# Optimization experiments

Hardware: AMD Instinct MI355X
Metric: run time of the kernel (lower is better)

## Reference

```python
import jax, jax.numpy as jnp
import numpy as np

HID = 1024       # hidden_size
H = 8            # num_attention_heads
KVH = 2          # num_key_value_heads
D = HID // H     # head_dim = 128
WINDOW = 2048    # sliding_window
THETA = 10000.0  # rope_theta
B, S = 1, 4096


def rotate_half(x):
    x1, x2 = jnp.split(x, 2, axis=-1)
    return jnp.concatenate([-x2, x1], axis=-1)


def setup_inputs() -> dict:
    key = jax.random.key(0)
    ks = jax.random.split(key, 5)
    scale = 0.02
    return {
        "hidden_states": jax.random.normal(ks[0], (B, S, HID), dtype=jnp.float32),
        "wq": jax.random.normal(ks[1], (H * D, HID), dtype=jnp.float32) * scale,
        "wk": jax.random.normal(ks[2], (KVH * D, HID), dtype=jnp.float32) * scale,
        "wv": jax.random.normal(ks[3], (KVH * D, HID), dtype=jnp.float32) * scale,
        "wo": jax.random.normal(ks[4], (HID, H * D), dtype=jnp.float32) * scale,
        "position_ids": jnp.broadcast_to(jnp.arange(S, dtype=jnp.int64 if jax.config.jax_enable_x64 else jnp.int32)[None, :], (B, S)),
    }


def reference(hidden_states, wq, wk, wv, wo, position_ids):
    b, s, _ = hidden_states.shape
    # projections (torch nn.Linear: x @ W^T)
    q = (hidden_states @ wq.T).reshape(b, s, H, D).transpose(0, 2, 1, 3)      # bhsd
    k = (hidden_states @ wk.T).reshape(b, s, KVH, D).transpose(0, 2, 1, 3)    # b(kv)sd
    v = (hidden_states @ wv.T).reshape(b, s, KVH, D).transpose(0, 2, 1, 3)

    # RoPE cache (head_dim, seq_len)
    inv_freq = 1.0 / THETA ** (jnp.arange(0, D, 2, dtype=jnp.float32) / D)
    t = jnp.arange(s, dtype=jnp.float32)
    freqs = t[:, None] * inv_freq[None, :]
    emb = jnp.concatenate([freqs, freqs], axis=-1)           # (S, D)
    cos = jnp.cos(emb)[position_ids][:, None]                # (B,1,S,D)
    sin = jnp.sin(emb)[position_ids][:, None]
    q = q * cos + rotate_half(q) * sin
    k = k * cos + rotate_half(k) * sin

    # GQA: repeat kv heads to match query heads (repeat_interleave on head dim)
    groups = H // KVH
    k = jnp.repeat(k, groups, axis=1)
    v = jnp.repeat(v, groups, axis=1)

    # full score matrix with sliding-window causal mask
    scores = jnp.einsum("bhqd,bhkd->bhqk", q, k)
    i = jnp.arange(s)[:, None]
    j = jnp.arange(s)[None, :]
    mask = (j <= i) & (j > i - WINDOW)                       # causal + window
    scores = jnp.where(mask[None, None], scores, -jnp.inf) / jnp.sqrt(jnp.float32(D))

    probs = jax.nn.softmax(scores.astype(jnp.float32), axis=-1).astype(q.dtype)
    ctx = jnp.einsum("bhqk,bhkd->bhqd", probs, v)
    ctx = ctx.transpose(0, 2, 1, 3).reshape(b, s, H * D)
    return ctx @ wo.T
```

## Files before the change

kernel.cpp:

```cpp
#include <hip/hip_runtime.h>

#define S_LEN 4096
#define HIDDEN 1024
#define NH 8
#define NKV 2
#define HD 128
#define WIN 2048

typedef short bf16x8 __attribute__((ext_vector_type(8)));
typedef short bf16x4 __attribute__((ext_vector_type(4)));
typedef float f32x4 __attribute__((ext_vector_type(4)));
typedef unsigned short u16x4 __attribute__((ext_vector_type(4)));

__device__ __forceinline__ unsigned short f2b(float f) {
    unsigned int u = __builtin_bit_cast(unsigned int, f);
    u += 0x7fffu + ((u >> 16) & 1u);
    return (unsigned short)(u >> 16);
}
__device__ __forceinline__ float b2f(unsigned short u) {
    unsigned int x = ((unsigned int)u) << 16;
    return __builtin_bit_cast(float, x);
}

__device__ __forceinline__ void gl_lds16(const unsigned short* g, unsigned short* l) {
    __builtin_amdgcn_global_load_lds(
        (const __attribute__((address_space(1))) unsigned int*)g,
        (__attribute__((address_space(3))) unsigned int*)l, 16, 0, 0);
}

#define WAIT_VM6   0x0F76
#define WAIT_VM0   0x0F70
#define MEMFENCE() __asm__ volatile("" ::: "memory")

__global__ __launch_bounds__(256) void cvt5(
    const float* __restrict__ s0, unsigned short* __restrict__ t0, int n0,
    const float* __restrict__ s1, unsigned short* __restrict__ t1, int n1,
    const float* __restrict__ s2, unsigned short* __restrict__ t2, int n2,
    const float* __restrict__ s3, unsigned short* __restrict__ t3, int n3,
    const float* __restrict__ s4, unsigned short* __restrict__ t4, int n4)
{
    int i = blockIdx.x * 256 + threadIdx.x;
    const float* s; unsigned short* t;
    if (i < n0)              { s = s0; t = t0; }
    else if ((i -= n0) < n1) { s = s1; t = t1; }
    else if ((i -= n1) < n2) { s = s2; t = t2; }
    else if ((i -= n2) < n3) { s = s3; t = t3; }
    else if ((i -= n3) < n4) { s = s4; t = t4; }
    else return;
    f32x4 v = *(const f32x4*)(s + (size_t)i * 4);
    u16x4 r = { f2b(v[0]), f2b(v[1]), f2b(v[2]), f2b(v[3]) };
    *(u16x4*)(t + (size_t)i * 4) = r;
}

__global__ __launch_bounds__(256, 2) void gemm128(
    const unsigned short* __restrict__ A, const unsigned short* __restrict__ W,
    float* __restrict__ Cf, unsigned short* __restrict__ Cb,
    int M, int N, int K)
{
    __shared__ alignas(16) unsigned short As[6][64 * 32];
    __shared__ alignas(16) unsigned short Bs[6][128 * 32];

    int lane = threadIdx.x & 63;
    int w = threadIdx.x >> 6;
    int l15 = lane & 15, quad = lane >> 4;

    int tiles_n = N >> 7;
    int bid = (int)blockIdx.x;
    int nb = (int)gridDim.x;
    int lb = bid;
    if ((nb & 7) == 0) {
        int c = nb >> 3;
        lb = (bid & 7) * c + (bid >> 3);
    }
    int mt0 = lb / tiles_n;
    int nt0 = lb - mt0 * tiles_n;

    size_t goffA;
    {
        int s = w * 64 + lane;
        int row = s >> 2, spos = s & 3;
        int kblk = spos ^ ((row >> 1) & 3);
        goffA = (size_t)(mt0 * 64 + row) * K + kblk * 8;
    }
    size_t goffB[2];
    #pragma unroll
    for (int is = 0; is < 2; ++is) {
        int s = w * 128 + is * 64 + lane;
        int row = s >> 2, spos = s & 3;
        int kblk = spos ^ ((row >> 1) & 3);
        goffB[is] = (size_t)(nt0 * 128 + row) * K + kblk * 8;
    }

    int arow0 = (w >> 1) * 32;
    int brow0 = (w & 1) * 64;
    int aoff[2], boff[4];
    #pragma unroll
    for (int t = 0; t < 2; ++t) {
        int ra = arow0 + t * 16 + l15;
        aoff[t] = (ra * 4 + (quad ^ ((ra >> 1) & 3))) * 8;
    }
    #pragma unroll
    for (int j = 0; j < 4; ++j) {
        int rb = brow0 + j * 16 + l15;
        boff[j] = (rb * 4 + (quad ^ ((rb >> 1) & 3))) * 8;
    }

    f32x4 acc[2][4];
    #pragma unroll
    for (int i = 0; i < 2; ++i)
        #pragma unroll
        for (int j = 0; j < 4; ++j) acc[i][j] = (f32x4){0.f, 0.f, 0.f, 0.f};

    auto stage = [&](int s, int b) {
        int k0 = s * 32;
        gl_lds16(A + goffA + k0, &As[b][(w * 64) * 8]);
        gl_lds16(W + goffB[0] + k0, &Bs[b][(w * 128 + 0) * 8]);
        gl_lds16(W + goffB[1] + k0, &Bs[b][(w * 128 + 64) * 8]);
    };

    int nk = K >> 5;
    int np = nk >> 1;
    if (nk > 0) stage(0, 0);
    if (nk > 1) stage(1, 1);
    if (nk > 2) stage(2, 2);
    if (nk > 3) stage(3, 3);
    int cb = 0, sb = 4;
    for (int j = 0; j < np; ++j) {
        MEMFENCE();
        if (j + 1 < np) __builtin_amdgcn_s_waitcnt(WAIT_VM6);
        else            __builtin_amdgcn_s_waitcnt(WAIT_VM0);
        __builtin_amdgcn_s_barrier();
        MEMFENCE();
        int s0 = 2 * j + 4;
        if (s0 < nk)     stage(s0, sb);
        if (s0 + 1 < nk) stage(s0 + 1, sb + 1 == 6 ? 0 : sb + 1);
        sb += 2; if (sb >= 6) sb -= 6;

        #pragma unroll
        for (int half = 0; half < 2; ++half) {
            const unsigned short* Ab = &As[cb + half][0];
            const unsigned short* Bb = &Bs[cb + half][0];
            bf16x8 af[2], bf_[4];
            #pragma unroll
            for (int t = 0; t < 2; ++t) af[t]  = *(const bf16x8*)(Ab + aoff[t]);
            #pragma unroll
            for (int jj = 0; jj < 4; ++jj) bf_[jj] = *(const bf16x8*)(Bb + boff[jj]);
            __builtin_amdgcn_s_setprio(1);
            #pragma unroll
            for (int i2 = 0; i2 < 2; ++i2)
                #pragma unroll
                for (int jj = 0; jj < 4; ++jj)
                    acc[i2][jj] = __builtin_amdgcn_mfma_f32_16x16x32_bf16(af[i2], bf_[jj], acc[i2][jj], 0, 0, 0);
            __builtin_amdgcn_s_setprio(0);
        }
        cb += 2; if (cb >= 6) cb -= 6;
        MEMFENCE();
    }

    #pragma unroll
    for (int i = 0; i < 2; ++i) {
        int row0 = mt0 * 64 + arow0 + i * 16 + quad * 4;
        #pragma unroll
        for (int j = 0; j < 4; ++j) {
            int col = nt0 * 128 + brow0 + j * 16 + l15;
            if (Cf) {
                #pragma unroll
                for (int reg = 0; reg < 4; ++reg)
                    Cf[(size_t)(row0 + reg) * N + col] = acc[i][j][reg];
            } else {
                #pragma unroll
                for (int reg = 0; reg < 4; ++reg)
                    Cb[(size_t)(row0 + reg) * N + col] = f2b(acc[i][j][reg]);
            }
        }
    }
}

#define QKVW (HIDDEN + 2 * NKV * HD)
__global__ __launch_bounds__(256, 2) void gemmqkv(
    const unsigned short* __restrict__ A, const unsigned short* __restrict__ W,
    const int* __restrict__ pos,
    unsigned short* __restrict__ Qb, unsigned short* __restrict__ Kb,
    unsigned short* __restrict__ Vt)
{
    __shared__ alignas(16) char pool[73728];
    unsigned short (*As)[64 * 32]  = (unsigned short (*)[64 * 32])(pool);
    unsigned short (*Bs)[128 * 32] = (unsigned short (*)[128 * 32])(pool + 24576);
    float (*Ex)[32][68] = (float (*)[32][68])(pool);
    unsigned short* T = (unsigned short*)(pool);

    int lane = threadIdx.x & 63;
    int w = threadIdx.x >> 6;
    int l15 = lane & 15, quad = lane >> 4;

    const int K = HIDDEN;
    int bid = (int)blockIdx.x;
    int lb = (bid & 7) * 96 + (bid >> 3);
    int mt0 = lb / 12;
    int nt0 = lb - mt0 * 12;

    size_t goffA;
    {
        int s = w * 64 + lane;
        int row = s >> 2, spos = s & 3;
        int kblk = spos ^ ((row >> 1) & 3);
        goffA = (size_t)(mt0 * 64 + row) * K + kblk * 8;
    }
    size_t goffB[2];
    #pragma unroll
    for (int is = 0; is < 2; ++is) {
        int s = w * 128 + is * 64 + lane;
        int row = s >> 2, spos = s & 3;
        int kblk = spos ^ ((row >> 1) & 3);
        goffB[is] = (size_t)(nt0 * 128 + row) * K + kblk * 8;
    }

    int arow0 = (w >> 1) * 32;
    int brow0 = (w & 1) * 64;
    int aoff[2], boff[4];
    #pragma unroll
    for (int t = 0; t < 2; ++t) {
        int ra = arow0 + t * 16 + l15;
        aoff[t] = (ra * 4 + (quad ^ ((ra >> 1) & 3))) * 8;
    }
    #pragma unroll
    for (int j = 0; j < 4; ++j) {
        int rb = brow0 + j * 16 + l15;
        boff[j] = (rb * 4 + (quad ^ ((rb >> 1) & 3))) * 8;
    }

    f32x4 acc[2][4];
    #pragma unroll
    for (int i = 0; i < 2; ++i)
        #pragma unroll
        for (int j = 0; j < 4; ++j) acc[i][j] = (f32x4){0.f, 0.f, 0.f, 0.f};

    auto stage = [&](int s, int b) {
        int k0 = s * 32;
        gl_lds16(A + goffA + k0, &As[b][(w * 64) * 8]);
        gl_lds16(W + goffB[0] + k0, &Bs[b][(w * 128 + 0) * 8]);
        gl_lds16(W + goffB[1] + k0, &Bs[b][(w * 128 + 64) * 8]);
    };

    stage(0, 0);
    stage(1, 1);
    stage(2, 2);
    stage(3, 3);
    int cb = 0, sb = 4;
    for (int j = 0; j < 16; ++j) {
        MEMFENCE();
        if (j < 15) __builtin_amdgcn_s_waitcnt(WAIT_VM6);
        else        __builtin_amdgcn_s_waitcnt(WAIT_VM0);
        __builtin_amdgcn_s_barrier();
        MEMFENCE();
        int s0 = 2 * j + 4;
        if (s0 < 32)     stage(s0, sb);
        if (s0 + 1 < 32) stage(s0 + 1, sb + 1 == 6 ? 0 : sb + 1);
        sb += 2; if (sb >= 6) sb -= 6;

        #pragma unroll
        for (int half = 0; half < 2; ++half) {
            const unsigned short* Ab = &As[cb + half][0];
            const unsigned short* Bb = &Bs[cb + half][0];
            bf16x8 af[2], bf_[4];
            #pragma unroll
            for (int t = 0; t < 2; ++t) af[t]  = *(const bf16x8*)(Ab + aoff[t]);
            #pragma unroll
            for (int jj = 0; jj < 4; ++jj) bf_[jj] = *(const bf16x8*)(Bb + boff[jj]);
            __builtin_amdgcn_s_setprio(1);
            #pragma unroll
            for (int i2 = 0; i2 < 2; ++i2)
                #pragma unroll
                for (int jj = 0; jj < 4; ++jj)
                    acc[i2][jj] = __builtin_amdgcn_mfma_f32_16x16x32_bf16(af[i2], bf_[jj], acc[i2][jj], 0, 0, 0);
            __builtin_amdgcn_s_setprio(0);
        }
        cb += 2; if (cb >= 6) cb -= 6;
        MEMFENCE();
    }

    if (nt0 >= 10) {
        int kv = nt0 - 10;
        __syncthreads();
        #pragma unroll
        for (int i = 0; i < 2; ++i) {
            int srow = arow0 + i * 16 + quad * 4;
            #pragma unroll
            for (int j = 0; j < 4; ++j) {
                int d = brow0 + j * 16 + l15;
                #pragma unroll
                for (int reg = 0; reg < 4; ++reg)
                    T[(srow + reg) * 130 + d] = f2b(acc[i][j][reg]);
            }
        }
        __syncthreads();
        int tid = threadIdx.x;
        int dl = tid >> 4;
        int s4 = (tid & 15) * 4;
        #pragma unroll
        for (int it = 0; it < 8; ++it) {
            int d = it * 16 + dl;
            u16x4 v4 = { T[(s4 + 0) * 130 + d], T[(s4 + 1) * 130 + d],
                         T[(s4 + 2) * 130 + d], T[(s4 + 3) * 130 + d] };
            *(u16x4*)(Vt + (size_t)kv * HD * S_LEN + (size_t)d * S_LEN
                      + mt0 * 64 + s4) = v4;
        }
        return;
    }

    bool isQ = (nt0 < 8);
    int kv = nt0 - 8;
    bool is64 = (pos[1] == 0) && (pos[3] == 0);
    const float qscale = 0.08838834764831843f;

    float invf[4];
    #pragma unroll
    for (int j = 0; j < 4; ++j) {
        int d6 = (brow0 + j * 16 + l15) & 63;
        invf[j] = exp2f(-(float)d6 * (13.287712379549449f / 64.0f));
    }

    __syncthreads();
    #pragma unroll
    for (int i = 0; i < 2; ++i)
        #pragma unroll
        for (int j = 0; j < 4; ++j)
            #pragma unroll
            for (int reg = 0; reg < 4; ++reg)
                Ex[w][i * 16 + quad * 4 + reg][j * 16 + l15] = acc[i][j][reg];
    __syncthreads();
    #pragma unroll
    for (int i = 0; i < 2; ++i) {
        #pragma unroll
        for (int reg = 0; reg < 4; ++reg) {
            int s = mt0 * 64 + arow0 + i * 16 + quad * 4 + reg;
            int pv_ = is64 ? pos[2 * s] : pos[s];
            float pf = (float)pv_;
            #pragma unroll
            for (int j = 0; j < 4; ++j) {
                float sn, cs;
                __sincosf(pf * invf[j], &sn, &cs);
                float a  = acc[i][j][reg];
                float pr = Ex[w ^ 1][i * 16 + quad * 4 + reg][j * 16 + l15];
                int d_local = brow0 + j * 16 + l15;
                float outv = (d_local < 64) ? (a * cs - pr * sn) : (a * cs + pr * sn);
                if (isQ) {
                    Qb[(size_t)s * HIDDEN + nt0 * HD + d_local] = f2b(outv * qscale);
                } else {
                    Kb[(size_t)kv * S_LEN * HD + (size_t)s * HD + d_local] = f2b(outv);
                }
            }
        }
    }
}

__global__ __launch_bounds__(256, 2) void attn_coop(
    const unsigned short* __restrict__ Qb, const unsigned short* __restrict__ Kb,
    const unsigned short* __restrict__ Vt, unsigned short* __restrict__ Ctx)
{
    __shared__ alignas(16) unsigned short Klds[2][64 * 128];
    __shared__ alignas(16) unsigned short Vlds[2][128 * 64];

    int lane = threadIdx.x & 63;
    int w = threadIdx.x >> 6;
    int l15 = lane & 15, quad = lane >> 4;
    int h = blockIdx.y;
    int kv = h >> 2;
    int qt = (h & 4) ? (63 - (int)blockIdx.x) : (int)blockIdx.x;
    int qb = qt * 64;
    int q16 = qb + w * 16;

    bf16x8 a_q[4];
    const unsigned short* qrow = Qb + (size_t)(q16 + l15) * HIDDEN + h * HD + quad * 8;
    #pragma unroll
    for (int st = 0; st < 4; ++st) a_q[st] = *(const bf16x8*)(qrow + st * 32);

    bf16x4 ones4;
    #pragma unroll
    for (int i = 0; i < 4; ++i) ones4[i] = (short)0x3F80;

    int lo = qb - (WIN - 1); if (lo < 0) lo = 0; lo &= ~63;
    int nch = (qb + 64 - lo) >> 6;

    const unsigned short* gbase;
    unsigned short* ldsdst[2];
    int myoff[8];
    int jmul;
    if (w < 2) {
        gbase = Kb + (size_t)kv * S_LEN * HD;
        ldsdst[0] = &Klds[0][w * 8 * 512];
        ldsdst[1] = &Klds[1][w * 8 * 512];
        jmul = HD;
        #pragma unroll
        for (int tt = 0; tt < 8; ++tt) {
            int t = w * 8 + tt;
            int key  = t * 4 + (lane >> 4);
            int dblk = (lane & 15) ^ (key & 15);
            myoff[tt] = key * HD + dblk * 8;
        }
    } else {
        gbase = Vt + (size_t)kv * HD * S_LEN;
        ldsdst[0] = &Vlds[0][(w - 2) * 8 * 512];
        ldsdst[1] = &Vlds[1][(w - 2) * 8 * 512];
        jmul = 1;
        #pragma unroll
        for (int tt = 0; tt < 8; ++tt) {
            int t = (w - 2) * 8 + tt;
            int d    = t * 8 + (lane >> 3);
            int kblk = (lane & 7) ^ (d & 7);
            myoff[tt] = d * S_LEN + kblk * 8;
        }
    }

    auto issue = [&](int c) {
        int j0 = lo + c * 64;
        const unsigned short* src = gbase + (size_t)j0 * jmul;
        unsigned short* dst = ldsdst[c & 1];
        #pragma unroll
        for (int tt = 0; tt < 8; ++tt)
            gl_lds16(src + myoff[tt], dst + tt * 512);
    };

    f32x4 o[9];
    #pragma unroll
    for (int nd = 0; nd < 9; ++nd) o[nd] = (f32x4){0.f, 0.f, 0.f, 0.f};

    issue(0);

    for (int c = 0; c < nch; ++c) {
        int j0 = lo + c * 64;

        MEMFENCE();
        __builtin_amdgcn_s_waitcnt(WAIT_VM0);
        __builtin_amdgcn_s_barrier();
        MEMFENCE();
        if (c + 1 < nch) issue(c + 1);

        const unsigned short* Kc = &Klds[c & 1][0];
        const unsigned short* Vc = &Vlds[c & 1][0];

        f32x4 sc[4];
        #pragma unroll
        for (int t = 0; t < 4; ++t) {
            sc[t] = (f32x4){0.f, 0.f, 0.f, 0.f};
            int key = t * 16 + l15;
            #pragma unroll
            for (int st = 0; st < 4; ++st) {
                int off16 = key * 16 + ((st * 4 + quad) ^ (key & 15));
                bf16x8 ak = *(const bf16x8*)(Kc + off16 * 8);
                sc[t] = __builtin_amdgcn_mfma_f32_16x16x32_bf16(ak, a_q[st], sc[t], 0, 0, 0);
            }
        }

        float p[4][4];
        if (j0 + 63 <= q16 && j0 > q16 + 15 - WIN) {
            #pragma unroll
            for (int t = 0; t < 4; ++t)
                #pragma unroll
                for (int reg = 0; reg < 4; ++reg) p[t][reg] = __expf(sc[t][reg]);
        } else {
            int iq = q16 + l15;
            #pragma unroll
            for (int t = 0; t < 4; ++t) {
                #pragma unroll
                for (int reg = 0; reg < 4; ++reg) {
                    int key = j0 + t * 16 + quad * 4 + reg;
                    p[t][reg] = (key <= iq && key > iq - WIN) ? __expf(sc[t][reg]) : 0.f;
                }
            }
        }

        bf16x4 a_p[4];
        #pragma unroll
        for (int t = 0; t < 4; ++t) {
            a_p[t][0] = (short)f2b(p[t][0]);
            a_p[t][1] = (short)f2b(p[t][1]);
            a_p[t][2] = (short)f2b(p[t][2]);
            a_p[t][3] = (short)f2b(p[t][3]);
        }

        #pragma unroll
        for (int t = 0; t < 4; ++t) {
            #pragma unroll
            for (int nd = 0; nd < 8; ++nd) {
                int d = nd * 16 + l15;
                int kblk = t * 2 + (quad >> 1);
                int slot = d * 8 + (kblk ^ (d & 7));
                bf16x4 bv = *(const bf16x4*)(Vc + slot * 8 + (quad & 1) * 4);
                o[nd] = __builtin_amdgcn_mfma_f32_16x16x16bf16_1k(a_p[t], bv, o[nd], 0, 0, 0);
            }
            o[8] = __builtin_amdgcn_mfma_f32_16x16x16bf16_1k(a_p[t], ones4, o[8], 0, 0, 0);
        }
        MEMFENCE();
    }

    #pragma unroll
    for (int nd = 0; nd < 8; ++nd) {
        int d = nd * 16 + l15;
        #pragma unroll
        for (int reg = 0; reg < 4; ++reg) {
            int q = q16 + quad * 4 + reg;
            Ctx[(size_t)q * HIDDEN + h * HD + d] = f2b(o[nd][reg] / o[8][reg]);
        }
    }
}

extern "C" void kernel_launch(void* const* d_in, const int* in_sizes, int n_in,
                              void* d_out, int out_size, void* d_ws, size_t ws_size,
                              hipStream_t stream)
{
    const float* hidden = (const float*)d_in[0];
    const float* wq = (const float*)d_in[1];
    const float* wk = (const float*)d_in[2];
    const float* wv = (const float*)d_in[3];
    const float* wo = (const float*)d_in[4];
    const int* pos = (const int*)d_in[5];
    float* out = (float*)d_out;

    char* ws = (char*)d_ws;
    size_t off = 0;
    unsigned short* Hb   = (unsigned short*)(ws + off); off += (size_t)S_LEN * HIDDEN * 2;
    unsigned short* Wqkv = (unsigned short*)(ws + off); off += (size_t)QKVW * HIDDEN * 2;
    unsigned short* Wob  = (unsigned short*)(ws + off); off += (size_t)HIDDEN * HIDDEN * 2;
    unsigned short* Qb   = (unsigned short*)(ws + off); off += (size_t)S_LEN * HIDDEN * 2;
    unsigned short* Kb   = (unsigned short*)(ws + off); off += (size_t)S_LEN * NKV * HD * 2;
    unsigned short* Vt   = (unsigned short*)(ws + off); off += (size_t)S_LEN * NKV * HD * 2;
    unsigned short* Cb   = (unsigned short*)(ws + off); off += (size_t)S_LEN * HIDDEN * 2;

    const int n_h  = S_LEN * HIDDEN / 4;
    const int n_wq = HIDDEN * HIDDEN / 4;
    const int n_wk = NKV * HD * HIDDEN / 4;
    int tot4 = n_h + n_wq + 2 * n_wk + n_wq;
    cvt5<<<(tot4 + 255) / 256, 256, 0, stream>>>(
        hidden, Hb, n_h,
        wq, Wqkv, n_wq,
        wk, Wqkv + (size_t)HIDDEN * HIDDEN, n_wk,
        wv, Wqkv + (size_t)(HIDDEN + NKV * HD) * HIDDEN, n_wk,
        wo, Wob, n_wq);

    gemmqkv<<<(S_LEN / 64) * 12, 256, 0, stream>>>(
        Hb, Wqkv, pos, Qb, Kb, Vt);

    attn_coop<<<dim3(S_LEN / 64, NH), 256, 0, stream>>>(Qb, Kb, Vt, Cb);

    gemm128<<<(S_LEN / 64) * (HIDDEN / 128), 256, 0, stream>>>(
        Cb, Wob, out, nullptr, S_LEN, HIDDEN, HIDDEN);
}
```

Measured before the change: 180.2 us.

## Fuse all four kernels into one persistent kernel with grid-wide barriers

```diff
diff --git a/kernel.cpp b/kernel.cpp
--- a/kernel.cpp
+++ b/kernel.cpp
@@ -32,475 +32,472 @@
 #define WAIT_VM0   0x0F70
 #define MEMFENCE() __asm__ volatile("" ::: "memory")
 
-__global__ __launch_bounds__(256) void cvt5(
-    const float* __restrict__ s0, unsigned short* __restrict__ t0, int n0,
-    const float* __restrict__ s1, unsigned short* __restrict__ t1, int n1,
-    const float* __restrict__ s2, unsigned short* __restrict__ t2, int n2,
-    const float* __restrict__ s3, unsigned short* __restrict__ t3, int n3,
-    const float* __restrict__ s4, unsigned short* __restrict__ t4, int n4)
+#define NBLK 512
+
+__device__ __forceinline__ void gsync(unsigned int* cnt) {
+    __syncthreads();
+    if (threadIdx.x == 0) {
+        __threadfence();
+        atomicAdd(cnt, 1u);
+        while (atomicAdd(cnt, 0u) < (unsigned)NBLK)
+            __builtin_amdgcn_s_sleep(2);
+        __threadfence();
+    }
+    __syncthreads();
+}
+
+#define QKVW (HIDDEN + 2 * NKV * HD)
+__global__ __launch_bounds__(256, 2) void fused(
+    const float* __restrict__ hidden, const float* __restrict__ wq,
+    const float* __restrict__ wk, const float* __restrict__ wv,
+    const float* __restrict__ wo, const int* __restrict__ pos,
+    unsigned short* __restrict__ Hb, unsigned short* __restrict__ Wqkv,
+    unsigned short* __restrict__ Wob, unsigned short* __restrict__ Qb,
+    unsigned short* __restrict__ Kb, unsigned short* __restrict__ Vt,
+    unsigned short* __restrict__ Cb, float* __restrict__ out,
+    unsigned int* __restrict__ sync)
 {
-    int i = blockIdx.x * 256 + threadIdx.x;
-    const float* s; unsigned short* t;
-    if (i < n0)              { s = s0; t = t0; }
-    else if ((i -= n0) < n1) { s = s1; t = t1; }
-    else if ((i -= n1) < n2) { s = s2; t = t2; }
-    else if ((i -= n2) < n3) { s = s3; t = t3; }
-    else if ((i -= n3) < n4) { s = s4; t = t4; }
-    else return;
-    f32x4 v = *(const f32x4*)(s + (size_t)i * 4);
-    u16x4 r = { f2b(v[0]), f2b(v[1]), f2b(v[2]), f2b(v[3]) };
-    *(u16x4*)(t + (size_t)i * 4) = r;
-}
-
-__global__ __launch_bounds__(256, 2) void gemm128(
-    const unsigned short* __restrict__ A, const unsigned short* __restrict__ W,
-    float* __restrict__ Cf, unsigned short* __restrict__ Cb,
-    int M, int N, int K)
-{
-    __shared__ alignas(16) unsigned short As[6][64 * 32];
-    __shared__ alignas(16) unsigned short Bs[6][128 * 32];
-
+    __shared__ alignas(16) char pool[73728];
+
+    int bid = (int)blockIdx.x;
     int lane = threadIdx.x & 63;
     int w = threadIdx.x >> 6;
     int l15 = lane & 15, quad = lane >> 4;
 
-    int tiles_n = N >> 7;
-    int bid = (int)blockIdx.x;
-    int nb = (int)gridDim.x;
-    int lb = bid;
-    if ((nb & 7) == 0) {
-        int c = nb >> 3;
-        lb = (bid & 7) * c + (bid >> 3);
+    {
+        const int n_h  = S_LEN * HIDDEN / 4;
+        const int n_wq = HIDDEN * HIDDEN / 4;
+        const int n_wk = NKV * HD * HIDDEN / 4;
+        const int tot4 = n_h + n_wq + 2 * n_wk + n_wq;
+        for (int i0 = bid * 256 + (int)threadIdx.x; i0 < tot4; i0 += NBLK * 256) {
+            int i = i0;
+            const float* s; unsigned short* t;
+            if (i < n_h)              { s = hidden; t = Hb; }
+            else if ((i -= n_h) < n_wq) { s = wq; t = Wqkv; }
+            else if ((i -= n_wq) < n_wk) { s = wk; t = Wqkv + (size_t)HIDDEN * HIDDEN; }
+            else if ((i -= n_wk) < n_wk) { s = wv; t = Wqkv + (size_t)(HIDDEN + NKV * HD) * HIDDEN; }
+            else { i -= n_wk; s = wo; t = Wob; }
+            f32x4 v = *(const f32x4*)(s + (size_t)i * 4);
+            u16x4 r = { f2b(v[0]), f2b(v[1]), f2b(v[2]), f2b(v[3]) };
+            *(u16x4*)(t + (size_t)i * 4) = r;
+        }
     }
-    int mt0 = lb / tiles_n;
-    int nt0 = lb - mt0 * tiles_n;
-
-    size_t goffA;
+    gsync(&sync[0]);
+
     {
-        int s = w * 64 + lane;
-        int row = s >> 2, spos = s & 3;
-        int kblk = spos ^ ((row >> 1) & 3);
-        goffA = (size_t)(mt0 * 64 + row) * K + kblk * 8;
+        unsigned short (*As)[64 * 32]  = (unsigned short (*)[64 * 32])(pool);
+        unsigned short (*Bs)[128 * 32] = (unsigned short (*)[128 * 32])(pool + 24576);
+        float (*Ex)[32][68] = (float (*)[32][68])(pool);
+        unsigned short* T = (unsigned short*)(pool);
+
+        const int K = HIDDEN;
+        int arow0 = (w >> 1) * 32;
+        int brow0 = (w & 1) * 64;
+        int aoff[2], boff[4];
+        #pragma unroll
+        for (int t = 0; t < 2; ++t) {
+            int ra = arow0 + t * 16 + l15;
+            aoff[t] = (ra * 4 + (quad ^ ((ra >> 1) & 3))) * 8;
+        }
+        #pragma unroll
+        for (int j = 0; j < 4; ++j) {
+            int rb = brow0 + j * 16 + l15;
+            boff[j] = (rb * 4 + (quad ^ ((rb >> 1) & 3))) * 8;
+        }
+        const float qscale = 0.08838834764831843f;
+        bool is64 = (pos[1] == 0) && (pos[3] == 0);
+
+        for (int tile = bid; tile < 768; tile += NBLK) {
+            __syncthreads();
+            int lb = (tile & 7) * 96 + (tile >> 3);
+            int mt0 = lb / 12;
+            int nt0 = lb - mt0 * 12;
+
+            size_t goffA;
+            {
+                int s = w * 64 + lane;
+                int row = s >> 2, spos = s & 3;
+                int kblk = spos ^ ((row >> 1) & 3);
+                goffA = (size_t)(mt0 * 64 + row) * K + kblk * 8;
+            }
+            size_t goffB[2];
+            #pragma unroll
+            for (int is = 0; is < 2; ++is) {
+                int s = w * 128 + is * 64 + lane;
+                int row = s >> 2, spos = s & 3;
+                int kblk = spos ^ ((row >> 1) & 3);
+                goffB[is] = (size_t)(nt0 * 128 + row) * K + kblk * 8;
+            }
+
+            f32x4 acc[2][4];
+            #pragma unroll
+            for (int i = 0; i < 2; ++i)
+                #pragma unroll
+                for (int j = 0; j < 4; ++j) acc[i][j] = (f32x4){0.f, 0.f, 0.f, 0.f};
+
+            auto stage = [&](int s, int b) {
+                int k0 = s * 32;
+                gl_lds16(Hb + goffA + k0, &As[b][(w * 64) * 8]);
+                gl_lds16(Wqkv + goffB[0] + k0, &Bs[b][(w * 128 + 0) * 8]);
+                gl_lds16(Wqkv + goffB[1] + k0, &Bs[b][(w * 128 + 64) * 8]);
+            };
+
+            stage(0, 0);
+            stage(1, 1);
+            stage(2, 2);
+            stage(3, 3);
+            int cb = 0, sb = 4;
+            for (int j = 0; j < 16; ++j) {
+                MEMFENCE();
+                if (j < 15) __builtin_amdgcn_s_waitcnt(WAIT_VM6);
+                else        __builtin_amdgcn_s_waitcnt(WAIT_VM0);
+                __builtin_amdgcn_s_barrier();
+                MEMFENCE();
+                int s0 = 2 * j + 4;
+                if (s0 < 32)     stage(s0, sb);
+                if (s0 + 1 < 32) stage(s0 + 1, sb + 1 == 6 ? 0 : sb + 1);
+                sb += 2; if (sb >= 6) sb -= 6;
+
+                #pragma unroll
+                for (int half = 0; half < 2; ++half) {
+                    const unsigned short* Ab = &As[cb + half][0];
+                    const unsigned short* Bb = &Bs[cb + half][0];
+                    bf16x8 af[2], bf_[4];
+                    #pragma unroll
+                    for (int t = 0; t < 2; ++t) af[t]  = *(const bf16x8*)(Ab + aoff[t]);
+                    #pragma unroll
+                    for (int jj = 0; jj < 4; ++jj) bf_[jj] = *(const bf16x8*)(Bb + boff[jj]);
+                    __builtin_amdgcn_s_setprio(1);
+                    #pragma unroll
+                    for (int i2 = 0; i2 < 2; ++i2)
+                        #pragma unroll
+                        for (int jj = 0; jj < 4; ++jj)
+                            acc[i2][jj] = __builtin_amdgcn_mfma_f32_16x16x32_bf16(af[i2], bf_[jj], acc[i2][jj], 0, 0, 0);
+                    __builtin_amdgcn_s_setprio(0);
+                }
+                cb += 2; if (cb >= 6) cb -= 6;
+                MEMFENCE();
+            }
+
+            if (nt0 >= 10) {
+                int kv = nt0 - 10;
+                __syncthreads();
+                #pragma unroll
+                for (int i = 0; i < 2; ++i) {
+                    int srow = arow0 + i * 16 + quad * 4;
+                    #pragma unroll
+                    for (int j = 0; j < 4; ++j) {
+                        int d = brow0 + j * 16 + l15;
+                        #pragma unroll
+                        for (int reg = 0; reg < 4; ++reg)
+                            T[(srow + reg) * 130 + d] = f2b(acc[i][j][reg]);
+                    }
+                }
+                __syncthreads();
+                int tid = threadIdx.x;
+                int dl = tid >> 4;
+                int s4 = (tid & 15) * 4;
+                #pragma unroll
+                for (int it = 0; it < 8; ++it) {
+                    int d = it * 16 + dl;
+                    u16x4 v4 = { T[(s4 + 0) * 130 + d], T[(s4 + 1) * 130 + d],
+                                 T[(s4 + 2) * 130 + d], T[(s4 + 3) * 130 + d] };
+                    *(u16x4*)(Vt + (size_t)kv * HD * S_LEN + (size_t)d * S_LEN
+                              + mt0 * 64 + s4) = v4;
+                }
+            } else {
+                bool isQ = (nt0 < 8);
+                int kv = nt0 - 8;
+                float invf[4];
+                #pragma unroll
+                for (int j = 0; j < 4; ++j) {
+                    int d6 = (brow0 + j * 16 + l15) & 63;
+                    invf[j] = exp2f(-(float)d6 * (13.287712379549449f / 64.0f));
+                }
+                __syncthreads();
+                #pragma unroll
+                for (int i = 0; i < 2; ++i)
+                    #pragma unroll
+                    for (int j = 0; j < 4; ++j)
+                        #pragma unroll
+                        for (int reg = 0; reg < 4; ++reg)
+                            Ex[w][i * 16 + quad * 4 + reg][j * 16 + l15] = acc[i][j][reg];
+                __syncthreads();
+                #pragma unroll
+                for (int i = 0; i < 2; ++i) {
+                    #pragma unroll
+                    for (int reg = 0; reg < 4; ++reg) {
+                        int s = mt0 * 64 + arow0 + i * 16 + quad * 4 + reg;
+                        int pv_ = is64 ? pos[2 * s] : pos[s];
+                        float pf = (float)pv_;
+                        #pragma unroll
+                        for (int j = 0; j < 4; ++j) {
+                            float sn, cs;
+                            __sincosf(pf * invf[j], &sn, &cs);
+                            float a  = acc[i][j][reg];
+                            float pr = Ex[w ^ 1][i * 16 + quad * 4 + reg][j * 16 + l15];
+                            int d_local = brow0 + j * 16 + l15;
+                            float outv = (d_local < 64) ? (a * cs - pr * sn) : (a * cs + pr * sn);
+                            if (isQ) {
+                                Qb[(size_t)s * HIDDEN + nt0 * HD + d_local] = f2b(outv * qscale);
+                            } else {
+                                Kb[(size_t)kv * S_LEN * HD + (size_t)s * HD + d_local] = f2b(outv);
+                            }
+                        }
+                    }
+                }
+            }
+        }
     }
-    size_t goffB[2];
-    #pragma unroll
-    for (int is = 0; is < 2; ++is) {
-        int s = w * 128 + is * 64 + lane;
-        int row = s >> 2, spos = s & 3;
-        int kblk = spos ^ ((row >> 1) & 3);
-        goffB[is] = (size_t)(nt0 * 128 + row) * K + kblk * 8;
+    gsync(&sync[1]);
+
+    {
+        unsigned short (*Klds)[64 * 128] = (unsigned short (*)[64 * 128])(pool);
+        unsigned short (*Vlds)[128 * 64] = (unsigned short (*)[128 * 64])(pool + 32768);
+
+        int h = bid >> 6;
+        int bx = bid & 63;
+        int kv = h >> 2;
+        int qt = (h & 4) ? (63 - bx) : bx;
+        int qb = qt * 64;
+        int q16 = qb + w * 16;
+
+        bf16x8 a_q[4];
+        const unsigned short* qrow = Qb + (size_t)(q16 + l15) * HIDDEN + h * HD + quad * 8;
+        #pragma unroll
+        for (int st = 0; st < 4; ++st) a_q[st] = *(const bf16x8*)(qrow + st * 32);
+
+        bf16x4 ones4;
+        #pragma unroll
+        for (int i = 0; i < 4; ++i) ones4[i] = (short)0x3F80;
+
+        int lo = qb - (WIN - 1); if (lo < 0) lo = 0; lo &= ~63;
+        int nch = (qb + 64 - lo) >> 6;
+
+        const unsigned short* gbase;
+        unsigned short* ldsdst[2];
+        int myoff[8];
+        int jmul;
+        if (w < 2) {
+            gbase = Kb + (size_t)kv * S_LEN * HD;
+            ldsdst[0] = &Klds[0][w * 8 * 512];
+            ldsdst[1] = &Klds[1][w * 8 * 512];
+            jmul = HD;
+            #pragma unroll
+            for (int tt = 0; tt < 8; ++tt) {
+                int t = w * 8 + tt;
+                int key  = t * 4 + (lane >> 4);
+                int dblk = (lane & 15) ^ (key & 15);
+                myoff[tt] = key * HD + dblk * 8;
+            }
+        } else {
+            gbase = Vt + (size_t)kv * HD * S_LEN;
+            ldsdst[0] = &Vlds[0][(w - 2) * 8 * 512];
+            ldsdst[1] = &Vlds[1][(w - 2) * 8 * 512];
+            jmul = 1;
+            #pragma unroll
+            for (int tt = 0; tt < 8; ++tt) {
+                int t = (w - 2) * 8 + tt;
+                int d    = t * 8 + (lane >> 3);
+                int kblk = (lane & 7) ^ (d & 7);
+                myoff[tt] = d * S_LEN + kblk * 8;
+            }
+        }
+
+        auto issue = [&](int c) {
+            int j0 = lo + c * 64;
+            const unsigned short* src = gbase + (size_t)j0 * jmul;
+            unsigned short* dst = ldsdst[c & 1];
+            #pragma unroll
+            for (int tt = 0; tt < 8; ++tt)
+                gl_lds16(src + myoff[tt], dst + tt * 512);
+        };
+
+        f32x4 o[9];
+        #pragma unroll
+        for (int nd = 0; nd < 9; ++nd) o[nd] = (f32x4){0.f, 0.f, 0.f, 0.f};
+
+        issue(0);
+
+        for (int c = 0; c < nch; ++c) {
+            int j0 = lo + c * 64;
+
+            MEMFENCE();
+            __builtin_amdgcn_s_waitcnt(WAIT_VM0);
+            __builtin_amdgcn_s_barrier();
+            MEMFENCE();
+            if (c + 1 < nch) issue(c + 1);
+
+            const unsigned short* Kc = &Klds[c & 1][0];
+            const unsigned short* Vc = &Vlds[c & 1][0];
+
+            f32x4 sc[4];
+            #pragma unroll
+            for (int t = 0; t < 4; ++t) {
+                sc[t] = (f32x4){0.f, 0.f, 0.f, 0.f};
+                int key = t * 16 + l15;
+                #pragma unroll
+                for (int st = 0; st < 4; ++st) {
+                    int off16 = key * 16 + ((st * 4 + quad) ^ (key & 15));
+                    bf16x8 ak = *(const bf16x8*)(Kc + off16 * 8);
+                    sc[t] = __builtin_amdgcn_mfma_f32_16x16x32_bf16(ak, a_q[st], sc[t], 0, 0, 0);
+                }
+            }
+
+            float p[4][4];
+            if (j0 + 63 <= q16 && j0 > q16 + 15 - WIN) {
+                #pragma unroll
+                for (int t = 0; t < 4; ++t)
+                    #pragma unroll
+                    for (int reg = 0; reg < 4; ++reg) p[t][reg] = __expf(sc[t][reg]);
+            } else {
+                int iq = q16 + l15;
+                #pragma unroll
+                for (int t = 0; t < 4; ++t) {
+                    #pragma unroll
+                    for (int reg = 0; reg < 4; ++reg) {
+                        int key = j0 + t * 16 + quad * 4 + reg;
+                        p[t][reg] = (key <= iq && key > iq - WIN) ? __expf(sc[t][reg]) : 0.f;
+                    }
+                }
+            }
+
+            bf16x4 a_p[4];
+            #pragma unroll
+            for (int t = 0; t < 4; ++t) {
+                a_p[t][0] = (short)f2b(p[t][0]);
+                a_p[t][1] = (short)f2b(p[t][1]);
+                a_p[t][2] = (short)f2b(p[t][2]);
+                a_p[t][3] = (short)f2b(p[t][3]);
+            }
+
+            #pragma unroll
+            for (int t = 0; t < 4; ++t) {
+                #pragma unroll
+                for (int nd = 0; nd < 8; ++nd) {
+                    int d = nd * 16 + l15;
+                    int kblk = t * 2 + (quad >> 1);
+                    int slot = d * 8 + (kblk ^ (d & 7));
+                    bf16x4 bv = *(const bf16x4*)(Vc + slot * 8 + (quad & 1) * 4);
+                    o[nd] = __builtin_amdgcn_mfma_f32_16x16x16bf16_1k(a_p[t], bv, o[nd], 0, 0, 0);
+                }
+                o[8] = __builtin_amdgcn_mfma_f32_16x16x16bf16_1k(a_p[t], ones4, o[8], 0, 0, 0);
+            }
+            MEMFENCE();
+        }
+
+        #pragma unroll
+        for (int nd = 0; nd < 8; ++nd) {
+            int d = nd * 16 + l15;
+            #pragma unroll
+            for (int reg = 0; reg < 4; ++reg) {
+                int q = q16 + quad * 4 + reg;
+                Cb[(size_t)q * HIDDEN + h * HD + d] = f2b(o[nd][reg] / o[8][reg]);
+            }
+        }
     }
-
-    int arow0 = (w >> 1) * 32;
-    int brow0 = (w & 1) * 64;
-    int aoff[2], boff[4];
-    #pragma unroll
-    for (int t = 0; t < 2; ++t) {
-        int ra = arow0 + t * 16 + l15;
-        aoff[t] = (ra * 4 + (quad ^ ((ra >> 1) & 3))) * 8;
-    }
-    #pragma unroll
-    for (int j = 0; j < 4; ++j) {
-        int rb = brow0 + j * 16 + l15;
-        boff[j] = (rb * 4 + (quad ^ ((rb >> 1) & 3))) * 8;
-    }
-
-    f32x4 acc[2][4];
-    #pragma unroll
-    for (int i = 0; i < 2; ++i)
-        #pragma unroll
-        for (int j = 0; j < 4; ++j) acc[i][j] = (f32x4){0.f, 0.f, 0.f, 0.f};
-
-    auto stage = [&](int s, int b) {
-        int k0 = s * 32;
-        gl_lds16(A + goffA + k0, &As[b][(w * 64) * 8]);
-        gl_lds16(W + goffB[0] + k0, &Bs[b][(w * 128 + 0) * 8]);
-        gl_lds16(W + goffB[1] + k0, &Bs[b][(w * 128 + 64) * 8]);
-    };
-
-    int nk = K >> 5;
-    int np = nk >> 1;
-    if (nk > 0) stage(0, 0);
-    if (nk > 1) stage(1, 1);
-    if (nk > 2) stage(2, 2);
-    if (nk > 3) stage(3, 3);
-    int cb = 0, sb = 4;
-    for (int j = 0; j < np; ++j) {
-        MEMFENCE();
-        if (j + 1 < np) __builtin_amdgcn_s_waitcnt(WAIT_VM6);
-        else            __builtin_amdgcn_s_waitcnt(WAIT_VM0);
-        __builtin_amdgcn_s_barrier();
-        MEMFENCE();
-        int s0 = 2 * j + 4;
-        if (s0 < nk)     stage(s0, sb);
-        if (s0 + 1 < nk) stage(s0 + 1, sb + 1 == 6 ? 0 : sb + 1);
-        sb += 2; if (sb >= 6) sb -= 6;
-
-        #pragma unroll
-        for (int half = 0; half < 2; ++half) {
-            const unsigned short* Ab = &As[cb + half][0];
-            const unsigned short* Bb = &Bs[cb + half][0];
-            bf16x8 af[2], bf_[4];
-            #pragma unroll
-            for (int t = 0; t < 2; ++t) af[t]  = *(const bf16x8*)(Ab + aoff[t]);
-            #pragma unroll
-            for (int jj = 0; jj < 4; ++jj) bf_[jj] = *(const bf16x8*)(Bb + boff[jj]);
-            __builtin_amdgcn_s_setprio(1);
-            #pragma unroll
-            for (int i2 = 0; i2 < 2; ++i2)
-                #pragma unroll
-                for (int jj = 0; jj < 4; ++jj)
-                    acc[i2][jj] = __builtin_amdgcn_mfma_f32_16x16x32_bf16(af[i2], bf_[jj], acc[i2][jj], 0, 0, 0);
-            __builtin_amdgcn_s_setprio(0);
-        }
-        cb += 2; if (cb >= 6) cb -= 6;
-        MEMFENCE();
-    }
-
-    #pragma unroll
-    for (int i = 0; i < 2; ++i) {
-        int row0 = mt0 * 64 + arow0 + i * 16 + quad * 4;
+    gsync(&sync[2]);
+
+    {
+        unsigned short (*As)[64 * 32]  = (unsigned short (*)[64 * 32])(pool);
+        unsigned short (*Bs)[128 * 32] = (unsigned short (*)[128 * 32])(pool + 24576);
+
+        const int K = HIDDEN, N = HIDDEN;
+        int lb = (bid & 7) * 64 + (bid >> 3);
+        int mt0 = lb >> 3;
+        int nt0 = lb & 7;
+
+        size_t goffA;
+        {
+            int s = w * 64 + lane;
+            int row = s >> 2, spos = s & 3;
+            int kblk = spos ^ ((row >> 1) & 3);
+            goffA = (size_t)(mt0 * 64 + row) * K + kblk * 8;
+        }
+        size_t goffB[2];
+        #pragma unroll
+        for (int is = 0; is < 2; ++is) {
+            int s = w * 128 + is * 64 + lane;
+            int row = s >> 2, spos = s & 3;
+            int kblk = spos ^ ((row >> 1) & 3);
+            goffB[is] = (size_t)(nt0 * 128 + row) * K + kblk * 8;
+        }
+
+        int arow0 = (w >> 1) * 32;
+        int brow0 = (w & 1) * 64;
+        int aoff[2], boff[4];
+        #pragma unroll
+        for (int t = 0; t < 2; ++t) {
+            int ra = arow0 + t * 16 + l15;
+            aoff[t] = (ra * 4 + (quad ^ ((ra >> 1) & 3))) * 8;
+        }
         #pragma unroll
         for (int j = 0; j < 4; ++j) {
-            int col = nt0 * 128 + brow0 + j * 16 + l15;
-            if (Cf) {
+            int rb = brow0 + j * 16 + l15;
+            boff[j] = (rb * 4 + (quad ^ ((rb >> 1) & 3))) * 8;
+        }
+
+        f32x4 acc[2][4];
+        #pragma unroll
+        for (int i = 0; i < 2; ++i)
+            #pragma unroll
+            for (int j = 0; j < 4; ++j) acc[i][j] = (f32x4){0.f, 0.f, 0.f, 0.f};
+
+        auto stage = [&](int s, int b) {
+            int k0 = s * 32;
+            gl_lds16(Cb + goffA + k0, &As[b][(w * 64) * 8]);
+            gl_lds16(Wob + goffB[0] + k0, &Bs[b][(w * 128 + 0) * 8]);
+            gl_lds16(Wob + goffB[1] + k0, &Bs[b][(w * 128 + 64) * 8]);
+        };
+
+        __syncthreads();
+        stage(0, 0);
+        stage(1, 1);
+        stage(2, 2);
+        stage(3, 3);
+        int cb = 0, sb = 4;
+        for (int j = 0; j < 16; ++j) {
+            MEMFENCE();
+            if (j < 15) __builtin_amdgcn_s_waitcnt(WAIT_VM6);
+            else        __builtin_amdgcn_s_waitcnt(WAIT_VM0);
+            __builtin_amdgcn_s_barrier();
+            MEMFENCE();
+            int s0 = 2 * j + 4;
+            if (s0 < 32)     stage(s0, sb);
+            if (s0 + 1 < 32) stage(s0 + 1, sb + 1 == 6 ? 0 : sb + 1);
+            sb += 2; if (sb >= 6) sb -= 6;
+
+            #pragma unroll
+            for (int half = 0; half < 2; ++half) {
+                const unsigned short* Ab = &As[cb + half][0];
+                const unsigned short* Bb = &Bs[cb + half][0];
+                bf16x8 af[2], bf_[4];
+                #pragma unroll
+                for (int t = 0; t < 2; ++t) af[t]  = *(const bf16x8*)(Ab + aoff[t]);
+                #pragma unroll
+                for (int jj = 0; jj < 4; ++jj) bf_[jj] = *(const bf16x8*)(Bb + boff[jj]);
+                __builtin_amdgcn_s_setprio(1);
+                #pragma unroll
+                for (int i2 = 0; i2 < 2; ++i2)
+                    #pragma unroll
+                    for (int jj = 0; jj < 4; ++jj)
+                        acc[i2][jj] = __builtin_amdgcn_mfma_f32_16x16x32_bf16(af[i2], bf_[jj], acc[i2][jj], 0, 0, 0);
+                __builtin_amdgcn_s_setprio(0);
+            }
+            cb += 2; if (cb >= 6) cb -= 6;
+            MEMFENCE();
+        }
+
+        #pragma unroll
+        for (int i = 0; i < 2; ++i) {
+            int row0 = mt0 * 64 + arow0 + i * 16 + quad * 4;
+            #pragma unroll
+            for (int j = 0; j < 4; ++j) {
+                int col = nt0 * 128 + brow0 + j * 16 + l15;
                 #pragma unroll
                 for (int reg = 0; reg < 4; ++reg)
-                    Cf[(size_t)(row0 + reg) * N + col] = acc[i][j][reg];
-            } else {
-                #pragma unroll
-                for (int reg = 0; reg < 4; ++reg)
-                    Cb[(size_t)(row0 + reg) * N + col] = f2b(acc[i][j][reg]);
-            }
-        }
-    }
-}
-
-#define QKVW (HIDDEN + 2 * NKV * HD)
-__global__ __launch_bounds__(256, 2) void gemmqkv(
-    const unsigned short* __restrict__ A, const unsigned short* __restrict__ W,
-    const int* __restrict__ pos,
-    unsigned short* __restrict__ Qb, unsigned short* __restrict__ Kb,
-    unsigned short* __restrict__ Vt)
-{
-    __shared__ alignas(16) char pool[73728];
-    unsigned short (*As)[64 * 32]  = (unsigned short (*)[64 * 32])(pool);
-    unsigned short (*Bs)[128 * 32] = (unsigned short (*)[128 * 32])(pool + 24576);
-    float (*Ex)[32][68] = (float (*)[32][68])(pool);
-    unsigned short* T = (unsigned short*)(pool);
-
-    int lane = threadIdx.x & 63;
-    int w = threadIdx.x >> 6;
-    int l15 = lane & 15, quad = lane >> 4;
-
-    const int K = HIDDEN;
-    int bid = (int)blockIdx.x;
-    int lb = (bid & 7) * 96 + (bid >> 3);
-    int mt0 = lb / 12;
-    int nt0 = lb - mt0 * 12;
-
-    size_t goffA;
-    {
-        int s = w * 64 + lane;
-        int row = s >> 2, spos = s & 3;
-        int kblk = spos ^ ((row >> 1) & 3);
-        goffA = (size_t)(mt0 * 64 + row) * K + kblk * 8;
-    }
-    size_t goffB[2];
-    #pragma unroll
-    for (int is = 0; is < 2; ++is) {
-        int s = w * 128 + is * 64 + lane;
-        int row = s >> 2, spos = s & 3;
-        int kblk = spos ^ ((row >> 1) & 3);
-        goffB[is] = (size_t)(nt0 * 128 + row) * K + kblk * 8;
-    }
-
-    int arow0 = (w >> 1) * 32;
-    int brow0 = (w & 1) * 64;
-    int aoff[2], boff[4];
-    #pragma unroll
-    for (int t = 0; t < 2; ++t) {
-        int ra = arow0 + t * 16 + l15;
-        aoff[t] = (ra * 4 + (quad ^ ((ra >> 1) & 3))) * 8;
-    }
-    #pragma unroll
-    for (int j = 0; j < 4; ++j) {
-        int rb = brow0 + j * 16 + l15;
-        boff[j] = (rb * 4 + (quad ^ ((rb >> 1) & 3))) * 8;
-    }
-
-    f32x4 acc[2][4];
-    #pragma unroll
-    for (int i = 0; i < 2; ++i)
-        #pragma unroll
-        for (int j = 0; j < 4; ++j) acc[i][j] = (f32x4){0.f, 0.f, 0.f, 0.f};
-
-    auto stage = [&](int s, int b) {
-        int k0 = s * 32;
-        gl_lds16(A + goffA + k0, &As[b][(w * 64) * 8]);
-        gl_lds16(W + goffB[0] + k0, &Bs[b][(w * 128 + 0) * 8]);
-        gl_lds16(W + goffB[1] + k0, &Bs[b][(w * 128 + 64) * 8]);
-    };
-
-    stage(0, 0);
-    stage(1, 1);
-    stage(2, 2);
-    stage(3, 3);
-    int cb = 0, sb = 4;
-    for (int j = 0; j < 16; ++j) {
-        MEMFENCE();
-        if (j < 15) __builtin_amdgcn_s_waitcnt(WAIT_VM6);
-        else        __builtin_amdgcn_s_waitcnt(WAIT_VM0);
-        __builtin_amdgcn_s_barrier();
-        MEMFENCE();
-        int s0 = 2 * j + 4;
-        if (s0 < 32)     stage(s0, sb);
-        if (s0 + 1 < 32) stage(s0 + 1, sb + 1 == 6 ? 0 : sb + 1);
-        sb += 2; if (sb >= 6) sb -= 6;
-
-        #pragma unroll
-        for (int half = 0; half < 2; ++half) {
-            const unsigned short* Ab = &As[cb + half][0];
-            const unsigned short* Bb = &Bs[cb + half][0];
-            bf16x8 af[2], bf_[4];
-            #pragma unroll
-            for (int t = 0; t < 2; ++t) af[t]  = *(const bf16x8*)(Ab + aoff[t]);
-            #pragma unroll
-            for (int jj = 0; jj < 4; ++jj) bf_[jj] = *(const bf16x8*)(Bb + boff[jj]);
-            __builtin_amdgcn_s_setprio(1);
-            #pragma unroll
-            for (int i2 = 0; i2 < 2; ++i2)
-                #pragma unroll
-                for (int jj = 0; jj < 4; ++jj)
-                    acc[i2][jj] = __builtin_amdgcn_mfma_f32_16x16x32_bf16(af[i2], bf_[jj], acc[i2][jj], 0, 0, 0);
-            __builtin_amdgcn_s_setprio(0);
-        }
-        cb += 2; if (cb >= 6) cb -= 6;
-        MEMFENCE();
-    }
-
-    if (nt0 >= 10) {
-        int kv = nt0 - 10;
-        __syncthreads();
-        #pragma unroll
-        for (int i = 0; i < 2; ++i) {
-            int srow = arow0 + i * 16 + quad * 4;
-            #pragma unroll
-            for (int j = 0; j < 4; ++j) {
-                int d = brow0 + j * 16 + l15;
-                #pragma unroll
-                for (int reg = 0; reg < 4; ++reg)
-                    T[(srow + reg) * 130 + d] = f2b(acc[i][j][reg]);
-            }
-        }
-        __syncthreads();
-        int tid = threadIdx.x;
-        int dl = tid >> 4;
-        int s4 = (tid & 15) * 4;
-        #pragma unroll
-        for (int it = 0; it < 8; ++it) {
-            int d = it * 16 + dl;
-            u16x4 v4 = { T[(s4 + 0) * 130 + d], T[(s4 + 1) * 130 + d],
-                         T[(s4 + 2) * 130 + d], T[(s4 + 3) * 130 + d] };
-            *(u16x4*)(Vt + (size_t)kv * HD * S_LEN + (size_t)d * S_LEN
-                      + mt0 * 64 + s4) = v4;
-        }
-        return;
-    }
-
-    bool isQ = (nt0 < 8);
-    int kv = nt0 - 8;
-    bool is64 = (pos[1] == 0) && (pos[3] == 0);
-    const float qscale = 0.08838834764831843f;
-
-    float invf[4];
-    #pragma unroll
-    for (int j = 0; j < 4; ++j) {
-        int d6 = (brow0 + j * 16 + l15) & 63;
-        invf[j] = exp2f(-(float)d6 * (13.287712379549449f / 64.0f));
-    }
-
-    __syncthreads();
-    #pragma unroll
-    for (int i = 0; i < 2; ++i)
-        #pragma unroll
-        for (int j = 0; j < 4; ++j)
-            #pragma unroll
-            for (int reg = 0; reg < 4; ++reg)
-                Ex[w][i * 16 + quad * 4 + reg][j * 16 + l15] = acc[i][j][reg];
-    __syncthreads();
-    #pragma unroll
-    for (int i = 0; i < 2; ++i) {
-        #pragma unroll
-        for (int reg = 0; reg < 4; ++reg) {
-            int s = mt0 * 64 + arow0 + i * 16 + quad * 4 + reg;
-            int pv_ = is64 ? pos[2 * s] : pos[s];
-            float pf = (float)pv_;
-            #pragma unroll
-            for (int j = 0; j < 4; ++j) {
-                float sn, cs;
-                __sincosf(pf * invf[j], &sn, &cs);
-                float a  = acc[i][j][reg];
-                float pr = Ex[w ^ 1][i * 16 + quad * 4 + reg][j * 16 + l15];
-                int d_local = brow0 + j * 16 + l15;
-                float outv = (d_local < 64) ? (a * cs - pr * sn) : (a * cs + pr * sn);
-                if (isQ) {
-                    Qb[(size_t)s * HIDDEN + nt0 * HD + d_local] = f2b(outv * qscale);
-                } else {
-                    Kb[(size_t)kv * S_LEN * HD + (size_t)s * HD + d_local] = f2b(outv);
-                }
-            }
-        }
-    }
-}
-
-__global__ __launch_bounds__(256, 2) void attn_coop(
-    const unsigned short* __restrict__ Qb, const unsigned short* __restrict__ Kb,
-    const unsigned short* __restrict__ Vt, unsigned short* __restrict__ Ctx)
-{
-    __shared__ alignas(16) unsigned short Klds[2][64 * 128];
-    __shared__ alignas(16) unsigned short Vlds[2][128 * 64];
-
-    int lane = threadIdx.x & 63;
-    int w = threadIdx.x >> 6;
-    int l15 = lane & 15, quad = lane >> 4;
-    int h = blockIdx.y;
-    int kv = h >> 2;
-    int qt = (h & 4) ? (63 - (int)blockIdx.x) : (int)blockIdx.x;
-    int qb = qt * 64;
-    int q16 = qb + w * 16;
-
-    bf16x8 a_q[4];
-    const unsigned short* qrow = Qb + (size_t)(q16 + l15) * HIDDEN + h * HD + quad * 8;
-    #pragma unroll
-    for (int st = 0; st < 4; ++st) a_q[st] = *(const bf16x8*)(qrow + st * 32);
-
-    bf16x4 ones4;
-    #pragma unroll
-    for (int i = 0; i < 4; ++i) ones4[i] = (short)0x3F80;
-
-    int lo = qb - (WIN - 1); if (lo < 0) lo = 0; lo &= ~63;
-    int nch = (qb + 64 - lo) >> 6;
-
-    const unsigned short* gbase;
-    unsigned short* ldsdst[2];
-    int myoff[8];
-    int jmul;
-    if (w < 2) {
-        gbase = Kb + (size_t)kv * S_LEN * HD;
-        ldsdst[0] = &Klds[0][w * 8 * 512];
-        ldsdst[1] = &Klds[1][w * 8 * 512];
-        jmul = HD;
-        #pragma unroll
-        for (int tt = 0; tt < 8; ++tt) {
-            int t = w * 8 + tt;
-            int key  = t * 4 + (lane >> 4);
-            int dblk = (lane & 15) ^ (key & 15);
-            myoff[tt] = key * HD + dblk * 8;
-        }
-    } else {
-        gbase = Vt + (size_t)kv * HD * S_LEN;
-        ldsdst[0] = &Vlds[0][(w - 2) * 8 * 512];
-        ldsdst[1] = &Vlds[1][(w - 2) * 8 * 512];
-        jmul = 1;
-        #pragma unroll
-        for (int tt = 0; tt < 8; ++tt) {
-            int t = (w - 2) * 8 + tt;
-            int d    = t * 8 + (lane >> 3);
-            int kblk = (lane & 7) ^ (d & 7);
-            myoff[tt] = d * S_LEN + kblk * 8;
-        }
-    }
-
-    auto issue = [&](int c) {
-        int j0 = lo + c * 64;
-        const unsigned short* src = gbase + (size_t)j0 * jmul;
-        unsigned short* dst = ldsdst[c & 1];
-        #pragma unroll
-        for (int tt = 0; tt < 8; ++tt)
-            gl_lds16(src + myoff[tt], dst + tt * 512);
-    };
-
-    f32x4 o[9];
-    #pragma unroll
-    for (int nd = 0; nd < 9; ++nd) o[nd] = (f32x4){0.f, 0.f, 0.f, 0.f};
-
-    issue(0);
-
-    for (int c = 0; c < nch; ++c) {
-        int j0 = lo + c * 64;
-
-        MEMFENCE();
-        __builtin_amdgcn_s_waitcnt(WAIT_VM0);
-        __builtin_amdgcn_s_barrier();
-        MEMFENCE();
-        if (c + 1 < nch) issue(c + 1);
-
-        const unsigned short* Kc = &Klds[c & 1][0];
-        const unsigned short* Vc = &Vlds[c & 1][0];
-
-        f32x4 sc[4];
-        #pragma unroll
-        for (int t = 0; t < 4; ++t) {
-            sc[t] = (f32x4){0.f, 0.f, 0.f, 0.f};
-            int key = t * 16 + l15;
-            #pragma unroll
-            for (int st = 0; st < 4; ++st) {
-                int off16 = key * 16 + ((st * 4 + quad) ^ (key & 15));
-                bf16x8 ak = *(const bf16x8*)(Kc + off16 * 8);
-                sc[t] = __builtin_amdgcn_mfma_f32_16x16x32_bf16(ak, a_q[st], sc[t], 0, 0, 0);
-            }
-        }
-
-        float p[4][4];
-        if (j0 + 63 <= q16 && j0 > q16 + 15 - WIN) {
-            #pragma unroll
-            for (int t = 0; t < 4; ++t)
-                #pragma unroll
-                for (int reg = 0; reg < 4; ++reg) p[t][reg] = __expf(sc[t][reg]);
-        } else {
-            int iq = q16 + l15;
-            #pragma unroll
-            for (int t = 0; t < 4; ++t) {
-                #pragma unroll
-                for (int reg = 0; reg < 4; ++reg) {
-                    int key = j0 + t * 16 + quad * 4 + reg;
-                    p[t][reg] = (key <= iq && key > iq - WIN) ? __expf(sc[t][reg]) : 0.f;
-                }
-            }
-        }
-
-        bf16x4 a_p[4];
-        #pragma unroll
-        for (int t = 0; t < 4; ++t) {
-            a_p[t][0] = (short)f2b(p[t][0]);
-            a_p[t][1] = (short)f2b(p[t][1]);
-            a_p[t][2] = (short)f2b(p[t][2]);
-            a_p[t][3] = (short)f2b(p[t][3]);
-        }
-
-        #pragma unroll
-        for (int t = 0; t < 4; ++t) {
-            #pragma unroll
-            for (int nd = 0; nd < 8; ++nd) {
-                int d = nd * 16 + l15;
-                int kblk = t * 2 + (quad >> 1);
-                int slot = d * 8 + (kblk ^ (d & 7));
-                bf16x4 bv = *(const bf16x4*)(Vc + slot * 8 + (quad & 1) * 4);
-                o[nd] = __builtin_amdgcn_mfma_f32_16x16x16bf16_1k(a_p[t], bv, o[nd], 0, 0, 0);
-            }
-            o[8] = __builtin_amdgcn_mfma_f32_16x16x16bf16_1k(a_p[t], ones4, o[8], 0, 0, 0);
-        }
-        MEMFENCE();
-    }
-
-    #pragma unroll
-    for (int nd = 0; nd < 8; ++nd) {
-        int d = nd * 16 + l15;
-        #pragma unroll
-        for (int reg = 0; reg < 4; ++reg) {
-            int q = q16 + quad * 4 + reg;
-            Ctx[(size_t)q * HIDDEN + h * HD + d] = f2b(o[nd][reg] / o[8][reg]);
+                    out[(size_t)(row0 + reg) * N + col] = acc[i][j][reg];
+            }
         }
     }
 }
@@ -526,23 +523,11 @@
     unsigned short* Kb   = (unsigned short*)(ws + off); off += (size_t)S_LEN * NKV * HD * 2;
     unsigned short* Vt   = (unsigned short*)(ws + off); off += (size_t)S_LEN * NKV * HD * 2;
     unsigned short* Cb   = (unsigned short*)(ws + off); off += (size_t)S_LEN * HIDDEN * 2;
-
-    const int n_h  = S_LEN * HIDDEN / 4;
-    const int n_wq = HIDDEN * HIDDEN / 4;
-    const int n_wk = NKV * HD * HIDDEN / 4;
-    int tot4 = n_h + n_wq + 2 * n_wk + n_wq;
-    cvt5<<<(tot4 + 255) / 256, 256, 0, stream>>>(
-        hidden, Hb, n_h,
-        wq, Wqkv, n_wq,
-        wk, Wqkv + (size_t)HIDDEN * HIDDEN, n_wk,
-        wv, Wqkv + (size_t)(HIDDEN + NKV * HD) * HIDDEN, n_wk,
-        wo, Wob, n_wq);
-
-    gemmqkv<<<(S_LEN / 64) * 12, 256, 0, stream>>>(
-        Hb, Wqkv, pos, Qb, Kb, Vt);
-
-    attn_coop<<<dim3(S_LEN / 64, NH), 256, 0, stream>>>(Qb, Kb, Vt, Cb);
-
-    gemm128<<<(S_LEN / 64) * (HIDDEN / 128), 256, 0, stream>>>(
-        Cb, Wob, out, nullptr, S_LEN, HIDDEN, HIDDEN);
+    unsigned int* sync   = (unsigned int*)(ws + off);   off += 64;
+
+    hipMemsetAsync(sync, 0, 64, stream);
+
+    fused<<<NBLK, 256, 0, stream>>>(
+        hidden, wq, wk, wv, wo, pos,
+        Hb, Wqkv, Wob, Qb, Kb, Vt, Cb, out, sync);
 }
```

Measured after the change: 331.3 us. +83.9%, slower.
